# Kernel tuning notes

Measured on AMD Instinct MI355X. Metric: run time of the kernel, lower is better.

## Reference

```python
import jax, jax.numpy as jnp
import numpy as np

B, S, D, H = 4, 2048, 768, 12
DH = D // H
SPARSITY = 0.5


def make_random_mask(key, seq_len, sparsity=SPARSITY):
    # Faithful to create_random_mask: uniform matrix, diagonal forced to 1,
    # top-k per row kept, diagonal forced on again.
    rand = jax.random.uniform(key, (seq_len, seq_len), dtype=jnp.float32)
    eye = jnp.eye(seq_len, dtype=bool)
    rand = jnp.where(eye, 1.0, rand)
    k = int(seq_len * (1.0 - sparsity))
    _, idx = jax.lax.top_k(rand, k)  # [S, k]
    mask = jnp.zeros((seq_len, seq_len), dtype=bool)
    rows = jnp.arange(seq_len)[:, None]
    mask = mask.at[rows, idx].set(True)
    mask = mask | eye
    return mask


def setup_inputs() -> dict:
    key = jax.random.key(0)
    ks = jax.random.split(key, 6)
    scale = 1.0 / np.sqrt(D)
    inp = {
        "hidden_states": jax.random.normal(ks[0], (B, S, D), dtype=jnp.float32),
        "Wq": jax.random.normal(ks[1], (D, D), dtype=jnp.float32) * scale,
        "bq": jnp.zeros((D,), dtype=jnp.float32),
        "Wk": jax.random.normal(ks[2], (D, D), dtype=jnp.float32) * scale,
        "bk": jnp.zeros((D,), dtype=jnp.float32),
        "Wv": jax.random.normal(ks[3], (D, D), dtype=jnp.float32) * scale,
        "bv": jnp.zeros((D,), dtype=jnp.float32),
        "Wo": jax.random.normal(ks[4], (D, D), dtype=jnp.float32) * scale,
        "bo": jnp.zeros((D,), dtype=jnp.float32),
        "random_mask": make_random_mask(ks[5], S),
    }
    return inp


def reference(hidden_states, Wq, bq, Wk, bk, Wv, bv, Wo, bo, random_mask):
    b, s, d = hidden_states.shape
    q = (hidden_states @ Wq + bq).reshape(b, s, H, DH).transpose(0, 2, 1, 3)  # [B,H,S,dH]
    k = (hidden_states @ Wk + bk).reshape(b, s, H, DH).transpose(0, 2, 1, 3)
    v = (hidden_states @ Wv + bv).reshape(b, s, H, DH).transpose(0, 2, 1, 3)

    scores = jnp.einsum('bhqd,bhkd->bhqk', q, k) / np.sqrt(DH)  # [B,H,S,S]
    scores = jnp.where(random_mask[None, None, :, :], scores, -1e9)
    probs = jax.nn.softmax(scores, axis=-1)
    ctx = jnp.einsum('bhqk,bhkd->bhqd', probs, v)  # [B,H,S,dH]
    ctx = ctx.transpose(0, 2, 1, 3).reshape(b, s, d)
    out = ctx @ Wo + bo
    return out
```

## Files before the change

kernel.cpp:

```cpp
#include <hip/hip_runtime.h>
#include <stdint.h>


#define B_ 4
#define S_ 2048
#define D_ 768
#define H_ 12
#define DH_ 64
#define NROW (B_ * S_)
#define MW (S_ / 64)

typedef __attribute__((ext_vector_type(4))) float f32x4;
typedef __attribute__((ext_vector_type(16))) float f32x16;
typedef __attribute__((ext_vector_type(8))) __bf16 bf16x8;
typedef __attribute__((ext_vector_type(8))) unsigned short us8;
typedef __attribute__((ext_vector_type(4))) unsigned short us4;
typedef __attribute__((ext_vector_type(2))) unsigned int u32x2;

#define LOG2E 1.4426950408889634f
#define SCQ (0.125f * LOG2E)

static __device__ __forceinline__ unsigned short f2bf(float f) {
  unsigned int u = __float_as_uint(f);
  unsigned int r = (u + 0x7fffu + ((u >> 16) & 1u)) >> 16;
  return (unsigned short)r;
}

static __device__ __forceinline__ unsigned int pk2c(float lo, float hi) {
  union { unsigned int u; __bf16 h[2]; } x;
  x.h[0] = (__bf16)lo; x.h[1] = (__bf16)hi;
  return x.u;
}

static __device__ __forceinline__ u32x2 swap32(unsigned int a, unsigned int b) {
  return __builtin_amdgcn_permlane32_swap(a, b, false, false);
}
static __device__ __forceinline__ float xhalf_sum(float x) {
  u32x2 r = swap32(__float_as_uint(x), __float_as_uint(x));
  return __uint_as_float(r[0]) + __uint_as_float(r[1]);
}

static __device__ __forceinline__ void gld_lds16(const void* g, void* l) {
  __builtin_amdgcn_global_load_lds(
      (const __attribute__((address_space(1))) void*)g,
      (__attribute__((address_space(3))) void*)l, 16, 0, 0);
}

#define PREP_CASTX 3072
#define PREP_TW 576
#define PREP_MB 2048
__global__ void k_prep(const float* __restrict__ hs,
                       const float* __restrict__ w0, const float* __restrict__ w1,
                       const float* __restrict__ w2, const float* __restrict__ w3,
                       const void* __restrict__ mask,
                       unsigned short* __restrict__ xb, unsigned short* __restrict__ wt,
                       unsigned long long* __restrict__ mb) {
  __shared__ float tl[64][65];
  int bid = blockIdx.x, t = threadIdx.x;

  if (bid < PREP_CASTX) {
    size_t i = (size_t)bid * 256 + t;
    const float4* p = (const float4*)(hs + i * 8);
    float4 a = p[0], b = p[1];
    us8 o;
    o[0] = f2bf(a.x); o[1] = f2bf(a.y); o[2] = f2bf(a.z); o[3] = f2bf(a.w);
    o[4] = f2bf(b.x); o[5] = f2bf(b.y); o[6] = f2bf(b.z); o[7] = f2bf(b.w);
    *(us8*)(xb + i * 8) = o;
  } else if (bid < PREP_CASTX + PREP_TW) {
    int tw = bid - PREP_CASTX;
    int z = tw / 144, r2 = tw % 144;
    int bx = r2 % 12, by = r2 / 12;
    const float* w = (z == 0) ? w0 : (z == 1) ? w1 : (z == 2) ? w2 : w3;
    int k0 = bx * 64, n0 = by * 64;
#pragma unroll
    for (int rr = 0; rr < 16; rr++) {
      int lin = rr * 256 + t;
      int kk = lin >> 6, nn = lin & 63;
      tl[kk][nn] = w[(size_t)(k0 + kk) * D_ + n0 + nn];
    }
    __syncthreads();
    unsigned short* o = wt + (size_t)z * D_ * D_;
#pragma unroll
    for (int rr = 0; rr < 16; rr++) {
      int lin = rr * 256 + t;
      int nn = lin >> 6, kk = lin & 63;
      o[(size_t)(n0 + nn) * D_ + k0 + kk] = f2bf(tl[kk][nn]);
    }
  } else {
    int mbid = bid - (PREP_CASTX + PREP_TW);
    int w = t >> 6, lane = t & 63;
    int base = mbid * 2048 + w * 512;
    int* sdet = (int*)tl;
    unsigned int wv[8];
#pragma unroll
    for (int j = 0; j < 8; j++) wv[j] = ((const unsigned int*)mask)[base + j * 64 + lane];
    int any = 0;
#pragma unroll
    for (int j = 0; j < 8; j++) any |= (wv[j] > 1u) ? 1 : 0;
    unsigned long long det = __ballot(any);
    if (lane == 0) sdet[w] = (det != 0ull);
    __syncthreads();
    int isbyte = sdet[0] | sdet[1] | sdet[2] | sdet[3];
    if (!isbyte) {
#pragma unroll
      for (int j = 0; j < 8; j++) {
        unsigned long long bw = __ballot(wv[j] != 0u);
        if (lane == 0) mb[mbid * 32 + w * 8 + j] = bw;
      }
    } else {
#pragma unroll
      for (int j = 0; j < 8; j++) {
        unsigned char bv = ((const unsigned char*)mask)[base + j * 64 + lane];
        unsigned long long bw = __ballot(bv != 0);
        if (lane == 0) mb[mbid * 32 + w * 8 + j] = bw;
      }
    }
  }
}

template <int MODE, typename OT>
static __device__ __forceinline__ void gemm_body(const unsigned short* __restrict__ A,
                                                 const unsigned short* __restrict__ Bt,
                                                 const float* __restrict__ bias,
                                                 OT* __restrict__ out) {
  __shared__ unsigned short As[128 * 32];
  __shared__ unsigned short Bs[128 * 32];
  int t = threadIdx.x;
  int lane = t & 63, wv = t >> 6;
  int wr = wv >> 1, wc = wv & 1;
  int c = lane & 15, g = lane >> 4;
  int rowBase = blockIdx.x * 128;
  int colBase = blockIdx.y * 128;

  f32x4 acc[4][4];
#pragma unroll
  for (int i = 0; i < 4; i++)
#pragma unroll
    for (int j = 0; j < 4; j++) acc[i][j] = {0.f, 0.f, 0.f, 0.f};

  for (int k0 = 0; k0 < D_; k0 += 32) {
    __syncthreads();
#pragma unroll
    for (int i = 0; i < 2; i++) {
      int p = t + i * 256;
      int row = p >> 2, u = p & 3;
      int ch = u ^ ((row >> 1) & 3);
      gld_lds16(A + (size_t)(rowBase + row) * D_ + k0 + ch * 8, &As[p * 8]);
      gld_lds16(Bt + (size_t)(colBase + row) * D_ + k0 + ch * 8, &Bs[p * 8]);
    }
    __syncthreads();
    bf16x8 af[4], bfr[4];
#pragma unroll
    for (int f = 0; f < 4; f++) {
      int row = wr * 64 + f * 16 + c;
      int ch = g ^ ((row >> 1) & 3);
      af[f] = *(const bf16x8*)&As[row * 32 + ch * 8];
      int col = wc * 64 + f * 16 + c;
      int ch2 = g ^ ((col >> 1) & 3);
      bfr[f] = *(const bf16x8*)&Bs[col * 32 + ch2 * 8];
    }
#pragma unroll
    for (int fi = 0; fi < 4; fi++)
#pragma unroll
      for (int fj = 0; fj < 4; fj++)
        acc[fi][fj] = __builtin_amdgcn_mfma_f32_16x16x32_bf16(af[fi], bfr[fj], acc[fi][fj], 0, 0, 0);
  }
  if constexpr (MODE == 2) {
#pragma unroll
    for (int fj = 0; fj < 4; fj++) {
      int col = colBase + wc * 64 + fj * 16 + c;
      float bv_ = bias[col];
      int hh = col >> 6, dh = col & 63;
#pragma unroll
      for (int fi = 0; fi < 4; fi++) {
        int row0 = rowBase + wr * 64 + fi * 16 + g * 4;
        int bb = row0 >> 11, sq = row0 & 2047;
        us4 pk;
#pragma unroll
        for (int r = 0; r < 4; r++) pk[r] = f2bf(acc[fi][fj][r] + bv_);
        *(us4*)&((unsigned short*)out)[(size_t)((bb * H_ + hh) * DH_ + dh) * S_ + sq] = pk;
      }
    }
  } else {
#pragma unroll
    for (int fj = 0; fj < 4; fj++) {
      int col = colBase + wc * 64 + fj * 16 + c;
      float bv_ = bias[col];
#pragma unroll
      for (int fi = 0; fi < 4; fi++) {
#pragma unroll
        for (int r = 0; r < 4; r++) {
          int row = rowBase + wr * 64 + fi * 16 + g * 4 + r;
          float v = acc[fi][fj][r] + bv_;
          if constexpr (MODE == 1) v *= SCQ;
          if constexpr (sizeof(OT) == 4) {
            ((float*)out)[(size_t)row * D_ + col] = v;
          } else {
            ((unsigned short*)out)[(size_t)row * D_ + col] = f2bf(v);
          }
        }
      }
    }
  }
}

__global__ void k_gemm_qkv(const unsigned short* __restrict__ X,
                           const unsigned short* __restrict__ Wt,
                           const float* __restrict__ bq, const float* __restrict__ bk,
                           const float* __restrict__ bv,
                           unsigned short* __restrict__ Q, unsigned short* __restrict__ K,
                           unsigned short* __restrict__ Vt_out) {
  int z = blockIdx.z;
  const unsigned short* Bt = Wt + (size_t)z * D_ * D_;
  if (z == 0)       gemm_body<1, unsigned short>(X, Bt, bq, Q);
  else if (z == 1)  gemm_body<0, unsigned short>(X, Bt, bk, K);
  else              gemm_body<2, unsigned short>(X, Bt, bv, Vt_out);
}

__global__ void k_gemm_out(const unsigned short* __restrict__ C,
                           const unsigned short* __restrict__ Wto,
                           const float* __restrict__ bo, float* __restrict__ out) {
  gemm_body<0, float>(C, Wto, bo, out);
}

__launch_bounds__(256, 4)
__global__ void k_attn(const unsigned short* __restrict__ Qn,
                       const unsigned short* __restrict__ Kn,
                       const unsigned short* __restrict__ Vt,
                       const unsigned long long* __restrict__ mb,
                       unsigned short* __restrict__ ctx) {
  __shared__ unsigned short Ks[2][64 * 64];
  __shared__ unsigned short Vs[2][64 * 64];

  int t = threadIdx.x;
  int lane = t & 63, w = t >> 6;
  int half = lane >> 5, lq = lane & 31;

  int wid = (blockIdx.x & 7) * 96 + (blockIdx.x >> 3);
  int qt = wid & 15, hb = wid >> 4;
  int h = hb % H_, b = hb / H_;
  int qbase = qt * 128, qw = w * 32;
  int mq = qbase + qw + lq;
  size_t qrow = (size_t)b * S_ + mq;

  const unsigned short* Kg = Kn + (size_t)b * S_ * D_ + h * DH_;
  const unsigned short* Vg = Vt + (size_t)((b * H_ + h) * DH_) * S_;

  bf16x8 qf[4];
#pragma unroll
  for (int ksl = 0; ksl < 4; ksl++)
    qf[ksl] = *(const bf16x8*)&Qn[qrow * D_ + h * DH_ + ksl * 16 + half * 8];

  f32x16 oacc[2];
#pragma unroll
  for (int j = 0; j < 16; j++) { oacc[0][j] = 0.f; oacc[1][j] = 0.f; }
  float l = 0.f;

  auto STAGE = [&](int nb, int kt2) {
    int kb2 = kt2 * 64;
#pragma unroll
    for (int i = 0; i < 2; i++) {
      int p = t + i * 256;
      int row = p >> 3, u = p & 7;
      int ch = u ^ (row & 7);
      gld_lds16(Kg + (size_t)(kb2 + row) * D_ + ch * 8, &Ks[nb][p * 8]);
      gld_lds16(Vg + (size_t)row * S_ + kb2 + ch * 8, &Vs[nb][p * 8]);
    }
  };

  STAGE(0, 0);
  unsigned long long mw = mb[(size_t)mq * MW];
  __syncthreads();

  int buf = 0;
  for (int kt = 0; kt < S_ / 64; kt++) {
    if (kt < S_ / 64 - 1) STAGE(buf ^ 1, kt + 1);
    unsigned long long mwu = mw;
    if (kt < S_ / 64 - 1) mw = mb[(size_t)mq * MW + kt + 1];

    f32x16 sacc[2];
#pragma unroll
    for (int j = 0; j < 16; j++) { sacc[0][j] = 0.f; sacc[1][j] = 0.f; }
#pragma unroll
    for (int sb = 0; sb < 2; sb++) {
      int kr = sb * 32 + lq;
      int sw = kr & 7;
#pragma unroll
      for (int ksl = 0; ksl < 4; ksl++) {
        int ch = (ksl * 2 + half) ^ sw;
        bf16x8 kf = *(const bf16x8*)&Ks[buf][kr * 64 + ch * 8];
        sacc[sb] = __builtin_amdgcn_mfma_f32_32x32x16_bf16(kf, qf[ksl], sacc[sb], 0, 0, 0);
      }
    }

    unsigned int msh0 = ((unsigned int)mwu) >> (4 * half);
    unsigned int msh1 = ((unsigned int)(mwu >> 32)) >> (4 * half);
    float psa[4] = {0.f, 0.f, 0.f, 0.f};
#pragma unroll
    for (int sb = 0; sb < 2; sb++) {
#pragma unroll
      for (int r = 0; r < 16; r++) {
        int cpos = (r & 3) + 8 * (r >> 2);
        unsigned int word = (sb == 0) ? msh0 : msh1;
        float e = __builtin_amdgcn_exp2f(sacc[sb][r]);
        e = ((word >> cpos) & 1u) ? e : 0.f;
        sacc[sb][r] = e;
        psa[r & 3] += e;
      }
    }
    l += (psa[0] + psa[1]) + (psa[2] + psa[3]);

    union PaU { unsigned int w[4]; bf16x8 v; } pa[4];
#pragma unroll
    for (int sb = 0; sb < 2; sb++)
#pragma unroll
      for (int par = 0; par < 2; par++) {
        int rb = par * 8;
        unsigned int x0 = pk2c(sacc[sb][rb + 0], sacc[sb][rb + 1]);
        unsigned int x1 = pk2c(sacc[sb][rb + 2], sacc[sb][rb + 3]);
        unsigned int y0 = pk2c(sacc[sb][rb + 4], sacc[sb][rb + 5]);
        unsigned int y1 = pk2c(sacc[sb][rb + 6], sacc[sb][rb + 7]);
        u32x2 r0 = swap32(x0, y0);
        u32x2 r1 = swap32(x1, y1);
        pa[sb * 2 + par].w[0] = r0[0];
        pa[sb * 2 + par].w[1] = r1[0];
        pa[sb * 2 + par].w[2] = r0[1];
        pa[sb * 2 + par].w[3] = r1[1];
      }

#pragma unroll
    for (int dhg = 0; dhg < 2; dhg++) {
      int dr = dhg * 32 + lq;
      int sw = lq & 7;
#pragma unroll
      for (int ks = 0; ks < 4; ks++) {
        int ch = (ks * 2 + half) ^ sw;
        bf16x8 vf = *(const bf16x8*)&Vs[buf][dr * 64 + ch * 8];
        oacc[dhg] = __builtin_amdgcn_mfma_f32_32x32x16_bf16(vf, pa[ks].v, oacc[dhg], 0, 0, 0);
      }
    }

    __syncthreads();
    buf ^= 1;
  }

  float linv = 1.0f / xhalf_sum(l);
  size_t obase = qrow * D_ + h * DH_;
#pragma unroll
  for (int dhg = 0; dhg < 2; dhg++)
#pragma unroll
    for (int i = 0; i < 4; i++) {
      us4 pk;
#pragma unroll
      for (int r = 0; r < 4; r++) pk[r] = f2bf(oacc[dhg][i * 4 + r] * linv);
      *(us4*)&ctx[obase + dhg * 32 + i * 8 + half * 4] = pk;
    }
}

extern "C" void kernel_launch(void* const* d_in, const int* in_sizes, int n_in,
                              void* d_out, int out_size, void* d_ws, size_t ws_size,
                              hipStream_t stream) {
  const float* hs = (const float*)d_in[0];
  const float* Wq = (const float*)d_in[1];
  const float* bq = (const float*)d_in[2];
  const float* Wk = (const float*)d_in[3];
  const float* bk = (const float*)d_in[4];
  const float* Wv = (const float*)d_in[5];
  const float* bv = (const float*)d_in[6];
  const float* Wo = (const float*)d_in[7];
  const float* bo = (const float*)d_in[8];
  const void* mask = d_in[9];
  float* out = (float*)d_out;

  char* ws = (char*)d_ws;
  size_t off = 0;
  auto alloc = [&](size_t bytes) -> void* {
    void* p = ws + off;
    off += (bytes + 255) & ~(size_t)255;
    return p;
  };
  unsigned short* Xb = (unsigned short*)alloc((size_t)NROW * D_ * 2);
  unsigned short* Wt = (unsigned short*)alloc((size_t)4 * D_ * D_ * 2);
  unsigned short* Qn = (unsigned short*)alloc((size_t)NROW * D_ * 2);
  unsigned short* Kn = (unsigned short*)alloc((size_t)NROW * D_ * 2);
  unsigned short* Vtr = (unsigned short*)alloc((size_t)B_ * H_ * DH_ * S_ * 2);
  unsigned short* Cx = (unsigned short*)alloc((size_t)NROW * D_ * 2);
  unsigned long long* Mb = (unsigned long long*)alloc((size_t)S_ * MW * 8);

  k_prep<<<PREP_CASTX + PREP_TW + PREP_MB, 256, 0, stream>>>(hs, Wq, Wk, Wv, Wo, mask, Xb, Wt, Mb);
  k_gemm_qkv<<<dim3(64, 6, 3), 256, 0, stream>>>(Xb, Wt, bq, bk, bv, Qn, Kn, Vtr);
  k_attn<<<768, 256, 0, stream>>>(Qn, Kn, Vtr, Mb, Cx);
  k_gemm_out<<<dim3(64, 6, 1), 256, 0, stream>>>(Cx, Wt + (size_t)3 * D_ * D_, bo, out);
}
```

Baseline: 256.3 us.

## Compute softmax row sums via MFMA with ones and remap GEMM blocks per XCD

Replaces the per-lane VALU accumulation of exponentiated scores (and the final cross-half permlane reduction) with an extra MFMA that multiplies a ones vector by the probability fragments, yielding row sums in a matrix accumulator. Also flattens the GEMM launch grids to 1D and remaps block ids so consecutive blocks on the same XCD share row tiles, aiming for better L2 reuse. The MFMA row sum adds four matrix instructions per key tile and 16 accumulator registers, and sums the bf16-rounded probabilities rather than the fp32 values.

Result: no change. 254.3 us (-0.8%).

```diff
diff --git a/kernel.cpp b/kernel.cpp
--- a/kernel.cpp
+++ b/kernel.cpp
@@ -34,10 +34,6 @@
 
 static __device__ __forceinline__ u32x2 swap32(unsigned int a, unsigned int b) {
   return __builtin_amdgcn_permlane32_swap(a, b, false, false);
-}
-static __device__ __forceinline__ float xhalf_sum(float x) {
-  u32x2 r = swap32(__float_as_uint(x), __float_as_uint(x));
-  return __uint_as_float(r[0]) + __uint_as_float(r[1]);
 }
 
 static __device__ __forceinline__ void gld_lds16(const void* g, void* l) {
@@ -122,15 +118,14 @@
 static __device__ __forceinline__ void gemm_body(const unsigned short* __restrict__ A,
                                                  const unsigned short* __restrict__ Bt,
                                                  const float* __restrict__ bias,
-                                                 OT* __restrict__ out) {
+                                                 OT* __restrict__ out,
+                                                 int rowBase, int colBase) {
   __shared__ unsigned short As[128 * 32];
   __shared__ unsigned short Bs[128 * 32];
   int t = threadIdx.x;
   int lane = t & 63, wv = t >> 6;
   int wr = wv >> 1, wc = wv & 1;
   int c = lane & 15, g = lane >> 4;
-  int rowBase = blockIdx.x * 128;
-  int colBase = blockIdx.y * 128;
 
   f32x4 acc[4][4];
 #pragma unroll
@@ -210,17 +205,24 @@
                            const float* __restrict__ bv,
                            unsigned short* __restrict__ Q, unsigned short* __restrict__ K,
                            unsigned short* __restrict__ Vt_out) {
-  int z = blockIdx.z;
+  int bid = blockIdx.x;
+  int bidp = (bid & 7) * 144 + (bid >> 3);
+  int x = bidp / 18, yz = bidp - x * 18;
+  int y = yz % 6, z = yz / 6;
+  int rowBase = x * 128, colBase = y * 128;
   const unsigned short* Bt = Wt + (size_t)z * D_ * D_;
-  if (z == 0)       gemm_body<1, unsigned short>(X, Bt, bq, Q);
-  else if (z == 1)  gemm_body<0, unsigned short>(X, Bt, bk, K);
-  else              gemm_body<2, unsigned short>(X, Bt, bv, Vt_out);
+  if (z == 0)       gemm_body<1, unsigned short>(X, Bt, bq, Q, rowBase, colBase);
+  else if (z == 1)  gemm_body<0, unsigned short>(X, Bt, bk, K, rowBase, colBase);
+  else              gemm_body<2, unsigned short>(X, Bt, bv, Vt_out, rowBase, colBase);
 }
 
 __global__ void k_gemm_out(const unsigned short* __restrict__ C,
                            const unsigned short* __restrict__ Wto,
                            const float* __restrict__ bo, float* __restrict__ out) {
-  gemm_body<0, float>(C, Wto, bo, out);
+  int bid = blockIdx.x;
+  int bidp = (bid & 7) * 48 + (bid >> 3);
+  int x = bidp / 6, y = bidp - x * 6;
+  gemm_body<0, float>(C, Wto, bo, out, x * 128, y * 128);
 }
 
 __launch_bounds__(256, 4)
@@ -251,10 +253,13 @@
   for (int ksl = 0; ksl < 4; ksl++)
     qf[ksl] = *(const bf16x8*)&Qn[qrow * D_ + h * DH_ + ksl * 16 + half * 8];
 
-  f32x16 oacc[2];
-#pragma unroll
-  for (int j = 0; j < 16; j++) { oacc[0][j] = 0.f; oacc[1][j] = 0.f; }
-  float l = 0.f;
+  union { us8 u; bf16x8 v; } ones_;
+#pragma unroll
+  for (int j = 0; j < 8; j++) ones_.u[j] = 0x3F80;
+
+  f32x16 oacc[2], lacc;
+#pragma unroll
+  for (int j = 0; j < 16; j++) { oacc[0][j] = 0.f; oacc[1][j] = 0.f; lacc[j] = 0.f; }
 
   auto STAGE = [&](int nb, int kt2) {
     int kb2 = kt2 * 64;
@@ -295,7 +300,6 @@
 
     unsigned int msh0 = ((unsigned int)mwu) >> (4 * half);
     unsigned int msh1 = ((unsigned int)(mwu >> 32)) >> (4 * half);
-    float psa[4] = {0.f, 0.f, 0.f, 0.f};
 #pragma unroll
     for (int sb = 0; sb < 2; sb++) {
 #pragma unroll
@@ -303,12 +307,9 @@
         int cpos = (r & 3) + 8 * (r >> 2);
         unsigned int word = (sb == 0) ? msh0 : msh1;
         float e = __builtin_amdgcn_exp2f(sacc[sb][r]);
-        e = ((word >> cpos) & 1u) ? e : 0.f;
-        sacc[sb][r] = e;
-        psa[r & 3] += e;
-      }
-    }
-    l += (psa[0] + psa[1]) + (psa[2] + psa[3]);
+        sacc[sb][r] = ((word >> cpos) & 1u) ? e : 0.f;
+      }
+    }
 
     union PaU { unsigned int w[4]; bf16x8 v; } pa[4];
 #pragma unroll
@@ -339,12 +340,15 @@
         oacc[dhg] = __builtin_amdgcn_mfma_f32_32x32x16_bf16(vf, pa[ks].v, oacc[dhg], 0, 0, 0);
       }
     }
+#pragma unroll
+    for (int ks = 0; ks < 4; ks++)
+      lacc = __builtin_amdgcn_mfma_f32_32x32x16_bf16(ones_.v, pa[ks].v, lacc, 0, 0, 0);
 
     __syncthreads();
     buf ^= 1;
   }
 
-  float linv = 1.0f / xhalf_sum(l);
+  float linv = 1.0f / lacc[0];
   size_t obase = qrow * D_ + h * DH_;
 #pragma unroll
   for (int dhg = 0; dhg < 2; dhg++)
@@ -388,7 +392,7 @@
   unsigned long long* Mb = (unsigned long long*)alloc((size_t)S_ * MW * 8);
 
   k_prep<<<PREP_CASTX + PREP_TW + PREP_MB, 256, 0, stream>>>(hs, Wq, Wk, Wv, Wo, mask, Xb, Wt, Mb);
-  k_gemm_qkv<<<dim3(64, 6, 3), 256, 0, stream>>>(Xb, Wt, bq, bk, bv, Qn, Kn, Vtr);
+  k_gemm_qkv<<<1152, 256, 0, stream>>>(Xb, Wt, bq, bk, bv, Qn, Kn, Vtr);
   k_attn<<<768, 256, 0, stream>>>(Qn, Kn, Vtr, Mb, Cx);
-  k_gemm_out<<<dim3(64, 6, 1), 256, 0, stream>>>(Cx, Wt + (size_t)3 * D_ * D_, bo, out);
-}
+  k_gemm_out<<<384, 256, 0, stream>>>(Cx, Wt + (size_t)3 * D_ * D_, bo, out);
+}
```
